# Kernel tuning notes

Hardware: AMD Instinct MI355X
Metric: run time of the kernel (lower is better)

The kernel has to match this reference:

```python
import jax, jax.numpy as jnp
import numpy as np

E = 8        # num_experts (material buckets)
L1 = 3072    # input dim
L2 = 15
L3 = 32
RF = 32      # ROUTER_FEATURES_PER_PERSPECTIVE
B = 16384
AUX_ALPHA = 0.01
Z_ALPHA = 0.001
LOAD_FLOOR = 0.05
LOAD_CAP = 0.5
PROBE_ALPHA = 0.01
PROBE_TAU = 1.0
PROBE_THRESH = 0.05
TEACHER_ALPHA = 0.0   # initial value of _teacher_alpha buffer
SCORE_SCALE = 600.0
SQ_SCALE = 255.0 / 256.0


def setup_inputs() -> dict:
    key = jax.random.key(0)
    ks = jax.random.split(key, 12)
    x = jax.random.uniform(ks[0], (B, L1), dtype=jnp.float32)
    ls_indices = jax.random.randint(ks[1], (B,), 0, E)
    psqt = jax.random.normal(ks[2], (B,), dtype=jnp.float32)
    score_target = jax.random.normal(ks[3], (B,), dtype=jnp.float32)
    router_w = 0.1 * jax.random.normal(ks[4], (E, 2 * RF), dtype=jnp.float32)
    router_b = jnp.zeros((E,), dtype=jnp.float32)
    # effective (coalesced) expert params, per _expert_params view
    w1 = jax.random.normal(ks[5], (E, L2 + 1, L1), dtype=jnp.float32) / np.sqrt(L1)
    b1 = 0.01 * jax.random.normal(ks[6], (E, L2 + 1), dtype=jnp.float32)
    w2 = jax.random.normal(ks[7], (E, L3, 2 * L2), dtype=jnp.float32) / np.sqrt(2 * L2)
    b2 = 0.01 * jax.random.normal(ks[8], (E, L3), dtype=jnp.float32)
    w3 = jax.random.normal(ks[9], (E, 1, L3), dtype=jnp.float32) / np.sqrt(L3)
    b3 = jnp.zeros((E, 1), dtype=jnp.float32)  # output bias zeroed in __init__
    return {"x": x, "ls_indices": ls_indices, "psqt": psqt,
            "score_target": score_target, "router_w": router_w,
            "router_b": router_b, "w1": w1, "b1": b1, "w2": w2, "b2": b2,
            "w3": w3, "b3": b3}


def _forward(x, psqt, score_target, router_w, router_b, w1, b1, w2, b2, w3, b3, ls_indices):
    half = L1 // 2
    router_in = jnp.concatenate([x[:, :RF], x[:, half:half + RF]], axis=1)  # [B, 64]
    gate_logits = router_in @ router_w.T + router_b                          # [B, E]
    logp = jax.nn.log_softmax(gate_logits, axis=-1)
    gate_probs = jnp.exp(logp)
    expert_indices = jnp.argmax(gate_logits, axis=-1)                        # [B]

    teacher_ce = -jnp.mean(jnp.take_along_axis(logp, ls_indices[:, None], axis=1))
    frac = jnp.bincount(expert_indices, length=E).astype(gate_probs.dtype) / gate_probs.shape[0]
    avg_gate = gate_probs.mean(axis=0)
    load = avg_gate + jax.lax.stop_gradient(frac - avg_gate)
    floor_loss = jnp.mean(jnp.square(jnp.maximum(LOAD_FLOOR - load, 0.0)))
    cap_loss = jnp.mean(jnp.square(jnp.maximum(load - LOAD_CAP, 0.0)))
    aux_loss = floor_loss + cap_loss
    z_loss = jnp.mean(jnp.square(jax.nn.logsumexp(gate_logits, axis=-1)))

    # ---- all-experts stacked MLP (fusion target) ----
    l1c = jnp.einsum('bi,eoi->beo', x, w1) + b1          # [B, E, L2+1]
    a, a_skip = l1c[..., :L2], l1c[..., L2:]              # [B,E,L2], [B,E,1]
    h = jnp.clip(jnp.concatenate([a * a * SQ_SCALE, a], axis=-1), 0.0, 1.0)  # [B,E,2*L2]
    l2x = jnp.clip(jnp.einsum('bei,eoi->beo', h, w2) + b2, 0.0, 1.0)         # [B,E,L3]
    all_out = jnp.einsum('bei,eoi->beo', l2x, w3) + b3 + a_skip              # [B,E,1]

    # ---- probe loss ----
    probe_weight = PROBE_ALPHA * max(PROBE_THRESH - TEACHER_ALPHA, 0.0) / max(PROBE_THRESH, 1e-9)
    expert_out = (all_out[..., 0] + psqt[:, None]) * SCORE_SCALE             # [B, E]
    err = jnp.square(expert_out - score_target[:, None])
    err = err - err.min(axis=1, keepdims=True)
    pt = jax.nn.softmax(-jax.lax.stop_gradient(err) / PROBE_TAU, axis=-1)
    log_pt = jnp.log(jnp.maximum(pt, 1e-30))
    probe_loss = jnp.mean(jnp.sum(pt * (log_pt - logp), axis=-1))            # kl_div batchmean

    router_loss = (AUX_ALPHA * aux_loss + Z_ALPHA * z_loss
                   + TEACHER_ALPHA * teacher_ce + probe_weight * probe_loss)

    l3x = jnp.take_along_axis(all_out, expert_indices[:, None, None], axis=1)[:, 0, :]  # [B, 1]
    gp = jnp.take_along_axis(gate_probs, expert_indices[:, None], axis=1)               # [B, 1]
    l3x = l3x * (1.0 + gp - jax.lax.stop_gradient(gp))  # straight-through (training mode)
    return l3x, router_loss


def reference(x, ls_indices, psqt, score_target, router_w, router_b, w1, b1, w2, b2, w3, b3):
    return _forward(x, psqt, score_target, router_w, router_b, w1, b1, w2, b2, w3, b3, ls_indices)
```

## Files before the change

### kernel.cpp

```cpp
#include <hip/hip_runtime.h>
#include <math.h>

#define BATCH 16384
#define K_DIM 3072

typedef float  f32x4  __attribute__((ext_vector_type(4)));
typedef __bf16 bf16x8 __attribute__((ext_vector_type(8)));
typedef unsigned int u32x2 __attribute__((ext_vector_type(2)));

__device__ __forceinline__ unsigned short f2bf(float f) {
  union { float f; unsigned u; } v; v.f = f;
  unsigned u = v.u + 0x7fffu + ((v.u >> 16) & 1u);
  return (unsigned short)(u >> 16);
}

__device__ __forceinline__ bf16x8 cvt8(f32x4 lo, f32x4 hi) {
  bf16x8 r;
  r[0] = (__bf16)lo[0]; r[1] = (__bf16)lo[1]; r[2] = (__bf16)lo[2]; r[3] = (__bf16)lo[3];
  r[4] = (__bf16)hi[0]; r[5] = (__bf16)hi[1]; r[6] = (__bf16)hi[2]; r[7] = (__bf16)hi[3];
  return r;
}

__device__ __forceinline__ void gld16(const void* g, void* l) {
  __builtin_amdgcn_global_load_lds(
      (const __attribute__((address_space(1))) unsigned int*)g,
      (__attribute__((address_space(3))) unsigned int*)l, 16, 0, 0);
}

__global__ void cvt_w1_kernel(const float* __restrict__ w1, unsigned short* __restrict__ o,
                              float* __restrict__ accs) {
  if (blockIdx.x == 0 && threadIdx.x < 16) accs[threadIdx.x] = 0.f;
  int i = blockIdx.x * 256 + threadIdx.x;
  f32x4 v = ((const f32x4*)w1)[i];
  u32x2 p = { (unsigned)f2bf(v.x) | ((unsigned)f2bf(v.y) << 16),
              (unsigned)f2bf(v.z) | ((unsigned)f2bf(v.w) << 16) };
  ((u32x2*)o)[i] = p;
}

__global__ __launch_bounds__(256, 2) void moe_main_kernel(
    const float* __restrict__ x, const unsigned short* __restrict__ w1bf,
    const float* __restrict__ b1, const float* __restrict__ w2,
    const float* __restrict__ b2, const float* __restrict__ w3,
    const float* __restrict__ b3, const float* __restrict__ psqt,
    const float* __restrict__ st, const float* __restrict__ rw,
    const float* __restrict__ rb, float* __restrict__ out,
    float* __restrict__ accs) {
  __shared__ __align__(16) unsigned char stage_sm[49152];
  __shared__ __align__(16) float w2s[8 * 964];
  __shared__ int   hist[8];
  __shared__ float zred[4], wred[4];

  const int tid = threadIdx.x;
  const int bm  = blockIdx.x;
  float* Cl = (float*)stage_sm;

  for (int i = tid; i < 7680; i += 256) {
    int e = i / 960; int r = i - e * 960; int o = r / 30; int ii = r - o * 30;
    w2s[e * 964 + ii * 32 + o] = w2[i];
  }
  if (tid < 8) hist[tid] = 0;
  __syncthreads();

  const int lane = tid & 63, wv = tid >> 6;
  const int l16 = lane & 15, lq = lane >> 4;
  const int rt = wv & 1;
  const int cb = (wv >> 1) << 2;

  const float* gA[2]; int lA[2];
#pragma unroll
  for (int r = 0; r < 2; ++r) {
    int idx = r * 256 + tid; int row = idx >> 4; int blk = idx & 15;
    gA[r] = x + (size_t)(bm * 32 + row) * K_DIM + ((blk ^ (row & 7)) << 2);
    lA[r] = idx << 4;
  }
  const unsigned short* gB[4]; int lB[4];
#pragma unroll
  for (int r = 0; r < 4; ++r) {
    int idx = r * 256 + tid; int row = idx >> 3; int blk = idx & 7;
    gB[r] = w1bf + (size_t)row * K_DIM + ((blk ^ (row & 7)) << 3);
    lB[r] = idx << 4;
  }

  const int arow = rt * 16 + l16;
  int aoff[2], boff[2][4];
#pragma unroll
  for (int ks = 0; ks < 2; ++ks) {
    aoff[ks] = arow * 256 + (((ks * 8 + lq * 2) ^ (arow & 7)) << 4);
#pragma unroll
    for (int cc = 0; cc < 4; ++cc) {
      int o = (cb + cc) * 16 + l16;
      boff[ks][cc] = o * 128 + (((lq + ks * 4) ^ (l16 & 7)) << 4);
    }
  }

#define STAGE(C, KT) do {                                                  \
    unsigned char* ab_ = stage_sm + (C) * 8192;                            \
    unsigned char* bb_ = stage_sm + 16384 + (C) * 16384;                   \
    gld16(gA[0] + (KT) * 64, ab_ + lA[0]);                                 \
    gld16(gA[1] + (KT) * 64, ab_ + lA[1]);                                 \
    gld16(gB[0] + (KT) * 64, bb_ + lB[0]);                                 \
    gld16(gB[1] + (KT) * 64, bb_ + lB[1]);                                 \
    gld16(gB[2] + (KT) * 64, bb_ + lB[2]);                                 \
    gld16(gB[3] + (KT) * 64, bb_ + lB[3]);                                 \
  } while (0)

#define COMPUTE(C) do {                                                    \
    const unsigned char* ab_ = stage_sm + (C) * 8192;                      \
    const unsigned char* bb_ = stage_sm + 16384 + (C) * 16384;             \
    _Pragma("unroll")                                                      \
    for (int ks = 0; ks < 2; ++ks) {                                       \
      f32x4 a0 = *(const f32x4*)(ab_ + aoff[ks]);                          \
      f32x4 a1 = *(const f32x4*)(ab_ + (aoff[ks] ^ 16));                   \
      bf16x8 af = cvt8(a0, a1);                                            \
      _Pragma("unroll")                                                    \
      for (int cc = 0; cc < 4; ++cc) {                                     \
        bf16x8 bfv = *(const bf16x8*)(bb_ + boff[ks][cc]);                 \
        acc[cc] = __builtin_amdgcn_mfma_f32_16x16x32_bf16(af, bfv,         \
                                                          acc[cc], 0,0,0); \
      }                                                                    \
    }                                                                      \
  } while (0)

  const int bl = tid >> 3, e = tid & 7;
  const int bg = bm * 32 + bl;
  const float* xrow  = x + (size_t)bg * K_DIM;
  const float* rwrow = rw + e * 64;
  double lr = (double)rb[e];
#pragma unroll
  for (int c4 = 0; c4 < 8; ++c4) {
    f32x4 xv = *(const f32x4*)(xrow + c4 * 4);
    f32x4 wvv = *(const f32x4*)(rwrow + c4 * 4);
#pragma unroll
    for (int j = 0; j < 4; ++j) lr = fma((double)xv[j], (double)wvv[j], lr);
  }
#pragma unroll
  for (int c4 = 0; c4 < 8; ++c4) {
    f32x4 xv = *(const f32x4*)(xrow + 1536 + c4 * 4);
    f32x4 wvv = *(const f32x4*)(rwrow + 32 + c4 * 4);
#pragma unroll
    for (int j = 0; j < 4; ++j) lr = fma((double)xv[j], (double)wvv[j], lr);
  }
  double mx = lr; int mi = e;
#pragma unroll
  for (int m = 1; m < 8; m <<= 1) {
    double ov = __shfl_xor(mx, m);
    int    oi = __shfl_xor(mi, m);
    if (ov > mx || (ov == mx && oi < mi)) { mx = ov; mi = oi; }
  }
  double ssum = exp(lr - mx);
#pragma unroll
  for (int m = 1; m < 8; m <<= 1) ssum += __shfl_xor(ssum, m);
  const double lse = mx + log(ssum);
  const float  logp_self = (float)(lr - lse);
  const int    rowEidx   = mi;

  if (e == 0) atomicAdd(&hist[rowEidx], 1);
  float zc = (e == 0) ? (float)(lse * lse) : 0.f;
#pragma unroll
  for (int m = 1; m < 64; m <<= 1) zc += __shfl_xor(zc, m);
  if (lane == 0) zred[wv] = zc;

  f32x4 acc[4];
#pragma unroll
  for (int cc = 0; cc < 4; ++cc) acc[cc] = (f32x4){0.f, 0.f, 0.f, 0.f};

  asm volatile("s_waitcnt vmcnt(0)" ::: "memory");
  STAGE(0, 0);

#pragma unroll 1
  for (int kt = 0; kt < 46; kt += 2) {
    STAGE(1, kt + 1);
    asm volatile("s_waitcnt vmcnt(6)" ::: "memory");
    __builtin_amdgcn_s_barrier();
    COMPUTE(0);
    __builtin_amdgcn_s_barrier();
    STAGE(0, kt + 2);
    asm volatile("s_waitcnt vmcnt(6)" ::: "memory");
    __builtin_amdgcn_s_barrier();
    COMPUTE(1);
    __builtin_amdgcn_s_barrier();
  }
  STAGE(1, 47);
  asm volatile("s_waitcnt vmcnt(6)" ::: "memory");
  __builtin_amdgcn_s_barrier();
  COMPUTE(0);
  __builtin_amdgcn_s_barrier();
  asm volatile("s_waitcnt vmcnt(0)" ::: "memory");
  __builtin_amdgcn_s_barrier();
  COMPUTE(1);
  __builtin_amdgcn_s_barrier();

#pragma unroll
  for (int cc = 0; cc < 4; ++cc)
#pragma unroll
    for (int r = 0; r < 4; ++r)
      Cl[(rt * 16 + lq * 4 + r) * 132 + (cb + cc) * 16 + l16] = acc[cc][r];
  __syncthreads();

  float a[16];
  {
    const float* crow = Cl + bl * 132 + e * 16;
    const float* b1p  = b1 + e * 16;
#pragma unroll
    for (int j = 0; j < 16; ++j) a[j] = crow[j] + b1p[j];
  }

  float h[30];
#pragma unroll
  for (int j = 0; j < 15; ++j) {
    float v = a[j];
    h[j]      = fminf(fmaxf(v * v * (255.0f / 256.0f), 0.f), 1.f);
    h[15 + j] = fminf(fmaxf(v, 0.f), 1.f);
  }

  float acc2[32];
  {
    const f32x4* b2v = (const f32x4*)(b2 + e * 32);
#pragma unroll
    for (int o4 = 0; o4 < 8; ++o4) {
      f32x4 t = b2v[o4];
      acc2[o4 * 4 + 0] = t.x; acc2[o4 * 4 + 1] = t.y;
      acc2[o4 * 4 + 2] = t.z; acc2[o4 * 4 + 3] = t.w;
    }
  }
  const f32x4* wrow = (const f32x4*)&w2s[e * 964];
#pragma unroll
  for (int i = 0; i < 30; ++i) {
    float hv = h[i];
#pragma unroll
    for (int o4 = 0; o4 < 8; ++o4) {
      f32x4 wq = wrow[i * 8 + o4];
      acc2[o4 * 4 + 0] += hv * wq.x;
      acc2[o4 * 4 + 1] += hv * wq.y;
      acc2[o4 * 4 + 2] += hv * wq.z;
      acc2[o4 * 4 + 3] += hv * wq.w;
    }
  }

  float outv = b3[e] + a[15];
  {
    const f32x4* w3v = (const f32x4*)(w3 + e * 32);
#pragma unroll
    for (int o4 = 0; o4 < 8; ++o4) {
      f32x4 t = w3v[o4];
      outv += fminf(fmaxf(acc2[o4 * 4 + 0], 0.f), 1.f) * t.x;
      outv += fminf(fmaxf(acc2[o4 * 4 + 1], 0.f), 1.f) * t.y;
      outv += fminf(fmaxf(acc2[o4 * 4 + 2], 0.f), 1.f) * t.z;
      outv += fminf(fmaxf(acc2[o4 * 4 + 3], 0.f), 1.f) * t.w;
    }
  }

  float eo  = (outv + psqt[bg]) * 600.0f;
  float dd  = eo - st[bg];
  float err = dd * dd;
  float mn = err;
  mn = fminf(mn, __shfl_xor(mn, 1));
  mn = fminf(mn, __shfl_xor(mn, 2));
  mn = fminf(mn, __shfl_xor(mn, 4));
  float wexp = expf(-(err - mn));
  float ss = wexp;
  ss += __shfl_xor(ss, 1); ss += __shfl_xor(ss, 2); ss += __shfl_xor(ss, 4);
  float pt  = wexp / ss;
  float lpt = logf(fmaxf(pt, 1e-30f));
  float term = pt * (lpt - logp_self);
  term += __shfl_xor(term, 1); term += __shfl_xor(term, 2); term += __shfl_xor(term, 4);
  float c1 = (e == 0) ? term : 0.f;
  c1 += __shfl_xor(c1, 8); c1 += __shfl_xor(c1, 16); c1 += __shfl_xor(c1, 32);
  if (lane == 0) wred[wv] = c1;

  if (e == rowEidx) out[bg] = outv;

  __syncthreads();
  if (tid == 0) {
    atomicAdd(&accs[8], zred[0] + zred[1] + zred[2] + zred[3]);
    atomicAdd(&accs[9], wred[0] + wred[1] + wred[2] + wred[3]);
  }
  if (tid < 8) atomicAdd(&accs[tid], (float)hist[tid]);
#undef STAGE
#undef COMPUTE
}

__global__ void finalize_kernel(const float* __restrict__ accs, float* __restrict__ out) {
  if (threadIdx.x == 0) {
    float fsum = 0.f;
    for (int e = 0; e < 8; ++e) {
      float frac = accs[e] * (1.0f / 16384.0f);
      float f = fmaxf(0.05f - frac, 0.f);
      float c = fmaxf(frac - 0.5f, 0.f);
      fsum += f * f + c * c;
    }
    float aux   = fsum * 0.125f;
    float z     = accs[8] * (1.0f / 16384.0f);
    float probe = accs[9] * (1.0f / 16384.0f);
    out[BATCH] = 0.01f * aux + 0.001f * z + 0.01f * probe;
  }
}

extern "C" void kernel_launch(void* const* d_in, const int* in_sizes, int n_in,
                              void* d_out, int out_size, void* d_ws, size_t ws_size,
                              hipStream_t stream) {
  const float* x    = (const float*)d_in[0];
  const float* psqt = (const float*)d_in[2];
  const float* st   = (const float*)d_in[3];
  const float* rw   = (const float*)d_in[4];
  const float* rb   = (const float*)d_in[5];
  const float* w1   = (const float*)d_in[6];
  const float* b1   = (const float*)d_in[7];
  const float* w2   = (const float*)d_in[8];
  const float* b2   = (const float*)d_in[9];
  const float* w3   = (const float*)d_in[10];
  const float* b3   = (const float*)d_in[11];
  float* out = (float*)d_out;

  unsigned short* w1bf = (unsigned short*)d_ws;
  float* accs = (float*)((char*)d_ws + 786432);

  cvt_w1_kernel<<<384, 256, 0, stream>>>(w1, w1bf, accs);
  moe_main_kernel<<<512, 256, 0, stream>>>(x, w1bf, b1, w2, b2, w3, b3,
                                           psqt, st, rw, rb, out, accs);
  finalize_kernel<<<1, 1, 0, stream>>>(accs, out);
}
```

Before: 333.2 us.

## Triple-buffer the K-loop staging and overlap router compute with prefetch

The GEMM staging moves from two LDS buffers to three, with each phase waiting only for the oldest stage so two tile loads stay in flight. The first two stages are issued before the router logit computation, so those loads overlap the router math. The w2 transpose into shared memory now happens after the GEMM, reusing the staging region, which keeps total LDS per block near its old size. The cost is more outstanding loads to track and a slightly longer epilogue.

```diff
diff --git a/kernel.cpp b/kernel.cpp
--- a/kernel.cpp
+++ b/kernel.cpp
@@ -45,19 +45,15 @@
     const float* __restrict__ st, const float* __restrict__ rw,
     const float* __restrict__ rb, float* __restrict__ out,
     float* __restrict__ accs) {
-  __shared__ __align__(16) unsigned char stage_sm[49152];
-  __shared__ __align__(16) float w2s[8 * 964];
+  __shared__ __align__(16) unsigned char stage_sm[73728];
   __shared__ int   hist[8];
   __shared__ float zred[4], wred[4];
 
   const int tid = threadIdx.x;
   const int bm  = blockIdx.x;
-  float* Cl = (float*)stage_sm;
-
-  for (int i = tid; i < 7680; i += 256) {
-    int e = i / 960; int r = i - e * 960; int o = r / 30; int ii = r - o * 30;
-    w2s[e * 964 + ii * 32 + o] = w2[i];
-  }
+  float* Cl  = (float*)stage_sm;
+  float* w2s = (float*)(stage_sm + 17024);
+
   if (tid < 8) hist[tid] = 0;
   __syncthreads();
 
@@ -94,8 +90,8 @@
   }
 
 #define STAGE(C, KT) do {                                                  \
-    unsigned char* ab_ = stage_sm + (C) * 8192;                            \
-    unsigned char* bb_ = stage_sm + 16384 + (C) * 16384;                   \
+    unsigned char* ab_ = stage_sm + (C) * 24576;                           \
+    unsigned char* bb_ = ab_ + 8192;                                       \
     gld16(gA[0] + (KT) * 64, ab_ + lA[0]);                                 \
     gld16(gA[1] + (KT) * 64, ab_ + lA[1]);                                 \
     gld16(gB[0] + (KT) * 64, bb_ + lB[0]);                                 \
@@ -105,8 +101,8 @@
   } while (0)
 
 #define COMPUTE(C) do {                                                    \
-    const unsigned char* ab_ = stage_sm + (C) * 8192;                      \
-    const unsigned char* bb_ = stage_sm + 16384 + (C) * 16384;             \
+    const unsigned char* ab_ = stage_sm + (C) * 24576;                     \
+    const unsigned char* bb_ = ab_ + 8192;                                 \
     _Pragma("unroll")                                                      \
     for (int ks = 0; ks < 2; ++ks) {                                       \
       f32x4 a0 = *(const f32x4*)(ab_ + aoff[ks]);                          \
@@ -121,6 +117,21 @@
     }                                                                      \
   } while (0)
 
+#define PH(C, T) do {                                                      \
+    STAGE(((C) + 2) % 3, (T) + 2);                                         \
+    asm volatile("s_waitcnt vmcnt(12)" ::: "memory");                      \
+    __builtin_amdgcn_s_barrier();                                          \
+    COMPUTE(C);                                                            \
+    __builtin_amdgcn_s_barrier();                                          \
+  } while (0)
+
+  f32x4 acc[4];
+#pragma unroll
+  for (int cc = 0; cc < 4; ++cc) acc[cc] = (f32x4){0.f, 0.f, 0.f, 0.f};
+
+  STAGE(0, 0);
+  STAGE(1, 1);
+
   const int bl = tid >> 3, e = tid & 7;
   const int bg = bm * 32 + bl;
   const float* xrow  = x + (size_t)bg * K_DIM;
@@ -160,34 +171,20 @@
   for (int m = 1; m < 64; m <<= 1) zc += __shfl_xor(zc, m);
   if (lane == 0) zred[wv] = zc;
 
-  f32x4 acc[4];
-#pragma unroll
-  for (int cc = 0; cc < 4; ++cc) acc[cc] = (f32x4){0.f, 0.f, 0.f, 0.f};
-
-  asm volatile("s_waitcnt vmcnt(0)" ::: "memory");
-  STAGE(0, 0);
-
 #pragma unroll 1
-  for (int kt = 0; kt < 46; kt += 2) {
-    STAGE(1, kt + 1);
-    asm volatile("s_waitcnt vmcnt(6)" ::: "memory");
-    __builtin_amdgcn_s_barrier();
-    COMPUTE(0);
-    __builtin_amdgcn_s_barrier();
-    STAGE(0, kt + 2);
-    asm volatile("s_waitcnt vmcnt(6)" ::: "memory");
-    __builtin_amdgcn_s_barrier();
-    COMPUTE(1);
-    __builtin_amdgcn_s_barrier();
-  }
-  STAGE(1, 47);
+  for (int kt = 0; kt < 45; kt += 3) {
+    PH(0, kt);
+    PH(1, kt + 1);
+    PH(2, kt + 2);
+  }
+  PH(0, 45);
   asm volatile("s_waitcnt vmcnt(6)" ::: "memory");
   __builtin_amdgcn_s_barrier();
-  COMPUTE(0);
+  COMPUTE(1);
   __builtin_amdgcn_s_barrier();
   asm volatile("s_waitcnt vmcnt(0)" ::: "memory");
   __builtin_amdgcn_s_barrier();
-  COMPUTE(1);
+  COMPUTE(2);
   __builtin_amdgcn_s_barrier();
 
 #pragma unroll
@@ -195,6 +192,10 @@
 #pragma unroll
     for (int r = 0; r < 4; ++r)
       Cl[(rt * 16 + lq * 4 + r) * 132 + (cb + cc) * 16 + l16] = acc[cc][r];
+  for (int i = tid; i < 7680; i += 256) {
+    int ee = i / 960; int rr = i - ee * 960; int o = rr / 30; int ii = rr - o * 30;
+    w2s[ee * 964 + ii * 32 + o] = w2[i];
+  }
   __syncthreads();
 
   float a[16];
@@ -278,6 +279,7 @@
   if (tid < 8) atomicAdd(&accs[tid], (float)hist[tid]);
 #undef STAGE
 #undef COMPUTE
+#undef PH
 }
 
 __global__ void finalize_kernel(const float* __restrict__ accs, float* __restrict__ out) {
```

After: 332.3 us. Within noise of the previous version (-0.3%).
